# Kernel tuning notes

Measured on AMD Instinct MI355X. Metric: run time of the kernel, lower is better.

The kernel has to match this reference:

```python
import jax, jax.numpy as jnp
import numpy as np

CROP_H, CROP_W = 14, 14


def _crop_and_resize_one_image(img, nboxes):
    """TF tf.image.crop_and_resize (bilinear, extrapolation_value=0) for one image.

    img: [H, W, C] float; nboxes: [N, 4] normalized (y1, x1, y2, x2).
    Returns [N, CROP_H, CROP_W, C].
    """
    H, W, C = img.shape
    dt = img.dtype
    y1, x1, y2, x2 = nboxes[:, 0], nboxes[:, 1], nboxes[:, 2], nboxes[:, 3]

    # Sample grid in pixel coordinates (crop size > 1 branch of TF op).
    ty = jnp.arange(CROP_H, dtype=dt) / (CROP_H - 1)  # [ch]
    tx = jnp.arange(CROP_W, dtype=dt) / (CROP_W - 1)  # [cw]
    ys = (y1[:, None] + (y2 - y1)[:, None] * ty[None, :]) * (H - 1)  # [N, ch]
    xs = (x1[:, None] + (x2 - x1)[:, None] * tx[None, :]) * (W - 1)  # [N, cw]

    valid_y = (ys >= 0) & (ys <= H - 1)  # [N, ch]
    valid_x = (xs >= 0) & (xs <= W - 1)  # [N, cw]

    y0f = jnp.floor(ys)
    x0f = jnp.floor(xs)
    wy = ys - y0f  # [N, ch]
    wx = xs - x0f  # [N, cw]
    y0 = jnp.clip(y0f, 0, H - 1).astype(jnp.int32)
    y1i = jnp.clip(y0f + 1, 0, H - 1).astype(jnp.int32)
    x0 = jnp.clip(x0f, 0, W - 1).astype(jnp.int32)
    x1i = jnp.clip(x0f + 1, 0, W - 1).astype(jnp.int32)

    def gather(yi, xi):  # yi [N,ch], xi [N,cw] -> [N,ch,cw,C]
        return img[yi[:, :, None], xi[:, None, :]]

    tl = gather(y0, x0)
    tr = gather(y0, x1i)
    bl = gather(y1i, x0)
    br = gather(y1i, x1i)

    wy_ = wy[:, :, None, None]
    wx_ = wx[:, None, :, None]
    out = (tl * (1 - wy_) * (1 - wx_) + tr * (1 - wy_) * wx_
           + bl * wy_ * (1 - wx_) + br * wy_ * wx_)

    mask = (valid_y[:, :, None] & valid_x[:, None, :])[..., None]
    return jnp.where(mask, out, jnp.zeros((), dtype=dt))


def setup_inputs() -> dict:
    key = jax.random.key(0)
    k1, k2, k3, k4, k5, k6 = jax.random.split(key, 6)
    B, N, H, W, C = 4, 256, 256, 256, 256
    # Boxes in pixel coordinates [x1, y1, x2, y2] with 0 <= x1 < x2 <= W etc.
    x1 = jax.random.uniform(k1, (B, N), minval=0.0, maxval=W / 2)
    y1 = jax.random.uniform(k2, (B, N), minval=0.0, maxval=H / 2)
    bw = jax.random.uniform(k3, (B, N), minval=4.0, maxval=W / 2)
    bh = jax.random.uniform(k4, (B, N), minval=4.0, maxval=H / 2)
    boxes = jnp.stack([x1, y1, x1 + bw, y1 + bh], axis=-1).astype(jnp.float32)
    fpn = jax.random.normal(k5, (B, H, W, C), dtype=jnp.float32)
    return {"boxes": boxes, "fpn": fpn}


def reference(boxes, fpn):
    boxes = jax.lax.stop_gradient(boxes)
    fpn = jax.lax.stop_gradient(fpn)
    B, H, W, C = fpn.shape
    Hf = jnp.asarray(H, dtype=fpn.dtype)
    Wf = jnp.asarray(W, dtype=fpn.dtype)

    x1 = boxes[..., 0]
    y1 = boxes[..., 1]
    x2 = boxes[..., 2]
    y2 = boxes[..., 3]
    # Exact normalization from the layer (image_shape == per-sample fpn shape).
    ny1 = y1 / Hf * Hf / (Hf - 1)
    nx1 = x1 / Wf * Wf / (Wf - 1)
    ny2 = (y2 / Hf * Hf - 1) / (Hf - 1)
    nx2 = (x2 / Wf * Wf - 1) / (Wf - 1)
    norm_boxes = jnp.stack([ny1, nx1, ny2, nx2], axis=-1)  # [B, N, 4]

    return jax.vmap(_crop_and_resize_one_image)(fpn, norm_boxes)
```

## Files before the change

### kernel.cpp

```cpp
#include <hip/hip_runtime.h>

constexpr int CROP_H = 14;
constexpr int CROP_W = 14;
constexpr int B = 4, N = 256, H = 256, W = 256, C = 256;

typedef float vfloat4 __attribute__((ext_vector_type(4)));

__global__ __launch_bounds__(256) void roi_align_kernel(
    const float* __restrict__ boxes,
    const float* __restrict__ fpn,
    float* __restrict__ out) {
  const int wave = threadIdx.x >> 6;
  const int lane = threadIdx.x & 63;
  int pos = blockIdx.x * 4 + wave;

  int j = pos % CROP_W;
  int t = pos / CROP_W;
  int i = t % CROP_H;
  t /= CROP_H;
  int n = t % N;
  int b = t / N;

  const float* bx = boxes + (size_t)(b * N + n) * 4;
  float x1 = bx[0], y1 = bx[1], x2 = bx[2], y2 = bx[3];

  const float Hf = (float)H, Wf = (float)W;
  float ny1 = y1 / Hf * Hf / (Hf - 1.0f);
  float nx1 = x1 / Wf * Wf / (Wf - 1.0f);
  float ny2 = (y2 / Hf * Hf - 1.0f) / (Hf - 1.0f);
  float nx2 = (x2 / Wf * Wf - 1.0f) / (Wf - 1.0f);

  float ty = (float)i / (float)(CROP_H - 1);
  float tx = (float)j / (float)(CROP_W - 1);
  float ys = (ny1 + (ny2 - ny1) * ty) * (Hf - 1.0f);
  float xs = (nx1 + (nx2 - nx1) * tx) * (Wf - 1.0f);

  bool valid = (ys >= 0.0f) && (ys <= Hf - 1.0f) &&
               (xs >= 0.0f) && (xs <= Wf - 1.0f);

  float y0f = floorf(ys), x0f = floorf(xs);
  float wy = ys - y0f, wx = xs - x0f;
  int y0  = (int)fminf(fmaxf(y0f,        0.0f), Hf - 1.0f);
  int y1i = (int)fminf(fmaxf(y0f + 1.0f, 0.0f), Hf - 1.0f);
  int x0  = (int)fminf(fmaxf(x0f,        0.0f), Wf - 1.0f);
  int x1i = (int)fminf(fmaxf(x0f + 1.0f, 0.0f), Wf - 1.0f);

  const float4* f4 = (const float4*)fpn;
  const int C4 = C >> 2;
  int rb = b * H;
  size_t i00 = (size_t)((rb + y0)  * W + x0)  * C4 + lane;
  size_t i01 = (size_t)((rb + y0)  * W + x1i) * C4 + lane;
  size_t i10 = (size_t)((rb + y1i) * W + x0)  * C4 + lane;
  size_t i11 = (size_t)((rb + y1i) * W + x1i) * C4 + lane;

  float4 tl = f4[i00];
  float4 tr = f4[i01];
  float4 bl = f4[i10];
  float4 br = f4[i11];

  float w00 = (1.0f - wy) * (1.0f - wx);
  float w01 = (1.0f - wy) * wx;
  float w10 = wy * (1.0f - wx);
  float w11 = wy * wx;

  vfloat4 o;
  o.x = tl.x * w00 + tr.x * w01 + bl.x * w10 + br.x * w11;
  o.y = tl.y * w00 + tr.y * w01 + bl.y * w10 + br.y * w11;
  o.z = tl.z * w00 + tr.z * w01 + bl.z * w10 + br.z * w11;
  o.w = tl.w * w00 + tr.w * w01 + bl.w * w10 + br.w * w11;
  if (!valid) { o.x = 0.0f; o.y = 0.0f; o.z = 0.0f; o.w = 0.0f; }

  vfloat4* dst = (vfloat4*)out + (size_t)pos * C4 + lane;
  __builtin_nontemporal_store(o, dst);
}

extern "C" void kernel_launch(void* const* d_in, const int* in_sizes, int n_in,
                              void* d_out, int out_size, void* d_ws, size_t ws_size,
                              hipStream_t stream) {
  const float* boxes = (const float*)d_in[0];
  const float* fpn   = (const float*)d_in[1];
  float* out = (float*)d_out;

  const int positions = B * N * CROP_H * CROP_W;
  dim3 grid(positions / 4), block(256);
  hipLaunchKernelGGL(roi_align_kernel, grid, block, 0, stream, boxes, fpn, out);
}
```

Before: 433.3 us.

## Add per-image prefetch blocks that stream the feature map into cache

The grid is reorganized so that each image gets 256 extra blocks, scheduled first at high priority. These blocks stream the whole 64MB image linearly so that the random bilinear gathers that follow hit in L2/MALL instead of DRAM. Gather blocks are also grouped per image for locality. The cost is roughly one extra full read of the fpn tensor plus more blocks, and a 64MB image may not fit in cache.

```diff
diff --git a/kernel.cpp b/kernel.cpp
--- a/kernel.cpp
+++ b/kernel.cpp
@@ -3,6 +3,12 @@
 constexpr int CROP_H = 14;
 constexpr int CROP_W = 14;
 constexpr int B = 4, N = 256, H = 256, W = 256, C = 256;
+constexpr int C4 = C / 4;
+constexpr int POS_PER_IMG = N * CROP_H * CROP_W;
+constexpr int GATHER_BLOCKS_PER_IMG = POS_PER_IMG / 4;
+constexpr int PREFETCH_BLOCKS_PER_IMG = 256;
+constexpr int BLOCKS_PER_IMG = GATHER_BLOCKS_PER_IMG + PREFETCH_BLOCKS_PER_IMG;
+constexpr size_t IMG_FLOAT4 = (size_t)H * W * C4;
 
 typedef float vfloat4 __attribute__((ext_vector_type(4)));
 
@@ -10,16 +16,35 @@
     const float* __restrict__ boxes,
     const float* __restrict__ fpn,
     float* __restrict__ out) {
+  const int b = blockIdx.x / BLOCKS_PER_IMG;
+  const int r = blockIdx.x % BLOCKS_PER_IMG;
+
+  if (r < PREFETCH_BLOCKS_PER_IMG) {
+    __builtin_amdgcn_s_setprio(3);
+    const float4* __restrict__ src =
+        (const float4*)fpn + (size_t)b * IMG_FLOAT4;
+    constexpr int CHUNK = (int)(IMG_FLOAT4 / PREFETCH_BLOCKS_PER_IMG);
+    const size_t base = (size_t)r * CHUNK + threadIdx.x;
+    float acc = 0.0f;
+#pragma unroll 4
+    for (int k = 0; k < CHUNK / 256; ++k) {
+      float4 v = src[base + (size_t)k * 256];
+      acc += v.x + v.y + v.z + v.w;
+    }
+    asm volatile("" :: "v"(acc));
+    __builtin_amdgcn_s_setprio(0);
+    return;
+  }
+
   const int wave = threadIdx.x >> 6;
   const int lane = threadIdx.x & 63;
-  int pos = blockIdx.x * 4 + wave;
+  const int p = (r - PREFETCH_BLOCKS_PER_IMG) * 4 + wave;
 
-  int j = pos % CROP_W;
-  int t = pos / CROP_W;
+  int j = p % CROP_W;
+  int t = p / CROP_W;
   int i = t % CROP_H;
-  t /= CROP_H;
-  int n = t % N;
-  int b = t / N;
+  int n = t / CROP_H;
+  const int pos = b * POS_PER_IMG + p;
 
   const float* bx = boxes + (size_t)(b * N + n) * 4;
   float x1 = bx[0], y1 = bx[1], x2 = bx[2], y2 = bx[3];
@@ -46,7 +71,6 @@
   int x1i = (int)fminf(fmaxf(x0f + 1.0f, 0.0f), Wf - 1.0f);
 
   const float4* f4 = (const float4*)fpn;
-  const int C4 = C >> 2;
   int rb = b * H;
   size_t i00 = (size_t)((rb + y0)  * W + x0)  * C4 + lane;
   size_t i01 = (size_t)((rb + y0)  * W + x1i) * C4 + lane;
@@ -81,7 +105,6 @@
   const float* fpn   = (const float*)d_in[1];
   float* out = (float*)d_out;
 
-  const int positions = B * N * CROP_H * CROP_W;
-  dim3 grid(positions / 4), block(256);
+  dim3 grid(B * BLOCKS_PER_IMG), block(256);
   hipLaunchKernelGGL(roi_align_kernel, grid, block, 0, stream, boxes, fpn, out);
 }
```

Measured after the change: 458.8 us. 5.9% more time.

## Sort crop rows by source image row for cache locality across XCDs

Applied to the files above, without the earlier changes.

Adds a single-block counting-sort kernel that orders (box, crop-row) items by their source image and row. The main kernel then reads positions through this permutation, with blocks interleaved so each XCD handles a contiguous span of sorted rows. The aim is to improve L2 reuse of gathered fpn rows, since each XCD has its own L2. The cost is an extra serial launch of one 1024-thread block plus scattered output writes, and the path only runs when a large enough workspace is supplied.

```diff
diff --git a/kernel.cpp b/kernel.cpp
--- a/kernel.cpp
+++ b/kernel.cpp
@@ -3,16 +3,88 @@
 constexpr int CROP_H = 14;
 constexpr int CROP_W = 14;
 constexpr int B = 4, N = 256, H = 256, W = 256, C = 256;
+constexpr int C4 = C / 4;
+constexpr int POSITIONS = B * N * CROP_H * CROP_W;
+constexpr int NBOXES = B * N;
+constexpr int ITEMS = NBOXES * CROP_H;
+constexpr int NBINS = B * H;
+constexpr int NXCD = 8;
+constexpr int POS_PER_XCD = POSITIONS / NXCD;
+constexpr size_t WS_NEEDED_BYTES = (size_t)ITEMS * 4;
 
 typedef float vfloat4 __attribute__((ext_vector_type(4)));
 
+__global__ __launch_bounds__(1024) void sort_rows_kernel(
+    const float* __restrict__ boxes, unsigned int* __restrict__ perm) {
+  __shared__ unsigned int cnt[NBINS];
+  __shared__ unsigned int wsum[16];
+  const int tid = threadIdx.x;
+  cnt[tid] = 0u;
+  __syncthreads();
+
+  const float* bx = boxes + (size_t)tid * 4;
+  const float y1 = bx[1], y2 = bx[3];
+  const float Hf = (float)H;
+  const float ny1 = y1 / Hf * Hf / (Hf - 1.0f);
+  const float ny2 = (y2 / Hf * Hf - 1.0f) / (Hf - 1.0f);
+  const int bimg = tid >> 8;
+
+  unsigned int mybin[CROP_H];
+#pragma unroll
+  for (int i = 0; i < CROP_H; ++i) {
+    float ty = (float)i / (float)(CROP_H - 1);
+    float ys = (ny1 + (ny2 - ny1) * ty) * (Hf - 1.0f);
+    float y0f = floorf(ys);
+    int y0 = (int)fminf(fmaxf(y0f, 0.0f), Hf - 1.0f);
+    mybin[i] = ((unsigned)bimg << 8) | (unsigned)y0;
+    atomicAdd(&cnt[mybin[i]], 1u);
+  }
+  __syncthreads();
+
+  unsigned c0 = cnt[tid];
+  unsigned v = c0;
+#pragma unroll
+  for (int d = 1; d < 64; d <<= 1) {
+    unsigned u = __shfl_up(v, d);
+    if ((tid & 63) >= d) v += u;
+  }
+  if ((tid & 63) == 63) wsum[tid >> 6] = v;
+  __syncthreads();
+  if (tid == 0) {
+    unsigned acc = 0;
+    for (int w = 0; w < 16; ++w) { unsigned t = wsum[w]; wsum[w] = acc; acc += t; }
+  }
+  __syncthreads();
+  cnt[tid] = v - c0 + wsum[tid >> 6];
+  __syncthreads();
+
+#pragma unroll
+  for (int i = 0; i < CROP_H; ++i) {
+    unsigned slot = atomicAdd(&cnt[mybin[i]], 1u);
+    perm[slot] = (unsigned)(tid * CROP_H + i);
+  }
+}
+
+template <bool USE_PERM>
 __global__ __launch_bounds__(256) void roi_align_kernel(
     const float* __restrict__ boxes,
     const float* __restrict__ fpn,
-    float* __restrict__ out) {
+    float* __restrict__ out,
+    const unsigned int* __restrict__ perm) {
   const int wave = threadIdx.x >> 6;
   const int lane = threadIdx.x & 63;
-  int pos = blockIdx.x * 4 + wave;
+
+  int pos;
+  if (USE_PERM) {
+    const int xcd = blockIdx.x & 7;
+    const int r   = blockIdx.x >> 3;
+    const unsigned slot = (unsigned)(xcd * POS_PER_XCD + r * 4 + wave);
+    const unsigned it = slot / 14u;
+    const unsigned jj = slot - it * 14u;
+    pos = (int)(perm[it] * 14u + jj);
+  } else {
+    pos = blockIdx.x * 4 + wave;
+  }
 
   int j = pos % CROP_W;
   int t = pos / CROP_W;
@@ -46,7 +118,6 @@
   int x1i = (int)fminf(fmaxf(x0f + 1.0f, 0.0f), Wf - 1.0f);
 
   const float4* f4 = (const float4*)fpn;
-  const int C4 = C >> 2;
   int rb = b * H;
   size_t i00 = (size_t)((rb + y0)  * W + x0)  * C4 + lane;
   size_t i01 = (size_t)((rb + y0)  * W + x1i) * C4 + lane;
@@ -81,7 +152,14 @@
   const float* fpn   = (const float*)d_in[1];
   float* out = (float*)d_out;
 
-  const int positions = B * N * CROP_H * CROP_W;
-  dim3 grid(positions / 4), block(256);
-  hipLaunchKernelGGL(roi_align_kernel, grid, block, 0, stream, boxes, fpn, out);
+  if (d_ws != nullptr && ws_size >= WS_NEEDED_BYTES) {
+    unsigned int* perm = (unsigned int*)d_ws;
+    hipLaunchKernelGGL(sort_rows_kernel, dim3(1), dim3(1024), 0, stream,
+                       boxes, perm);
+    hipLaunchKernelGGL(roi_align_kernel<true>, dim3(POSITIONS / 4), dim3(256),
+                       0, stream, boxes, fpn, out, perm);
+  } else {
+    hipLaunchKernelGGL(roi_align_kernel<false>, dim3(POSITIONS / 4), dim3(256),
+                       0, stream, boxes, fpn, out, (const unsigned int*)nullptr);
+  }
 }
```

After: 430.7 us. No clear change (-0.6%).
